# Optimization experiments

Measured on AMD Instinct MI355X. Metric: run time of the kernel, lower is better.

## Reference

```python
import jax, jax.numpy as jnp
import numpy as np

FP8_MAX = 448.0
EPS = 1e-12


def setup_inputs() -> dict:
    key = jax.random.key(0)
    k1, k2 = jax.random.split(key)
    x = jax.random.normal(k1, (4, 2048, 4096), dtype=jnp.float32)
    # kaiming-uniform-like init scale for weight
    weight = jax.random.normal(k2, (4096, 4096), dtype=jnp.float32) * 0.02
    bias = jnp.zeros((4096,), dtype=jnp.float32)
    return {"x": x, "weight": weight, "bias": bias}


def reference(x, weight, bias):
    # per-tensor fake-quant of activations
    input_scale = jnp.maximum(jnp.max(jnp.abs(x)) / FP8_MAX, EPS)
    x_q = jnp.round(jnp.clip(x / input_scale, -FP8_MAX, FP8_MAX))
    # per-tensor fake-quant of weight
    weight_scale = jnp.maximum(jnp.max(jnp.abs(weight)) / FP8_MAX, EPS)
    weight_q = jnp.round(jnp.clip(weight / weight_scale, -FP8_MAX, FP8_MAX))
    # GEMM in quantized domain, then dequant rescale + bias
    out_q = jnp.einsum('bsi,oi->bso', x_q, weight_q)  # [B,S,out]
    out = (out_q * (input_scale * weight_scale)).astype(x.dtype) + bias
    return out
```

## Files before the change

kernel.cpp:

```cpp
#include <hip/hip_runtime.h>

#define FP8_MAX 448.0f
#define EPSF 1e-12f

#define BM 256
#define BN 256
#define BK 64

typedef __attribute__((ext_vector_type(8))) _Float16 half8;
typedef __attribute__((ext_vector_type(4))) float floatx4;

__device__ inline void async_copy16(const void* gp, void* lp) {
  __builtin_amdgcn_global_load_lds(
      (const __attribute__((address_space(1))) unsigned int*)gp,
      (__attribute__((address_space(3))) unsigned int*)lp,
      16, 0, 0);
}

__global__ void absmax_kernel(const float* __restrict__ in, int n4,
                              unsigned* __restrict__ out) {
  int tid = blockIdx.x * blockDim.x + threadIdx.x;
  int stride = gridDim.x * blockDim.x;
  const float4* in4 = (const float4*)in;
  float m = 0.f;
  for (int i = tid; i < n4; i += stride) {
    float4 v = in4[i];
    m = fmaxf(m, fmaxf(fmaxf(fabsf(v.x), fabsf(v.y)),
                       fmaxf(fabsf(v.z), fabsf(v.w))));
  }
  for (int off = 32; off > 0; off >>= 1)
    m = fmaxf(m, __shfl_down(m, off, 64));
  __shared__ float smax[4];
  int lane = threadIdx.x & 63, w = threadIdx.x >> 6;
  if (lane == 0) smax[w] = m;
  __syncthreads();
  if (threadIdx.x == 0) {
    float b = fmaxf(fmaxf(smax[0], smax[1]), fmaxf(smax[2], smax[3]));
    atomicMax(out, __float_as_uint(b));
  }
}

__global__ void quant_kernel(const float* __restrict__ in,
                             _Float16* __restrict__ out, int n8,
                             const unsigned* __restrict__ amax_bits) {
  const float scale = fmaxf(__uint_as_float(*amax_bits) / FP8_MAX, EPSF);
  int tid = blockIdx.x * blockDim.x + threadIdx.x;
  int stride = gridDim.x * blockDim.x;
  const float4* in4 = (const float4*)in;
  half8* out8 = (half8*)out;
  for (int i = tid; i < n8; i += stride) {
    float4 a = in4[2 * i], b = in4[2 * i + 1];
    half8 h;
    h[0] = (_Float16)rintf(fminf(fmaxf(a.x / scale, -FP8_MAX), FP8_MAX));
    h[1] = (_Float16)rintf(fminf(fmaxf(a.y / scale, -FP8_MAX), FP8_MAX));
    h[2] = (_Float16)rintf(fminf(fmaxf(a.z / scale, -FP8_MAX), FP8_MAX));
    h[3] = (_Float16)rintf(fminf(fmaxf(a.w / scale, -FP8_MAX), FP8_MAX));
    h[4] = (_Float16)rintf(fminf(fmaxf(b.x / scale, -FP8_MAX), FP8_MAX));
    h[5] = (_Float16)rintf(fminf(fmaxf(b.y / scale, -FP8_MAX), FP8_MAX));
    h[6] = (_Float16)rintf(fminf(fmaxf(b.z / scale, -FP8_MAX), FP8_MAX));
    h[7] = (_Float16)rintf(fminf(fmaxf(b.w / scale, -FP8_MAX), FP8_MAX));
    out8[i] = h;
  }
}

__global__ __launch_bounds__(512, 2) void gemm8_kernel(
    const _Float16* __restrict__ A,
    const _Float16* __restrict__ B,
    const float* __restrict__ bias, const unsigned* __restrict__ amax,
    float* __restrict__ C,
    int M, int N, int K) {
  __shared__ __align__(16) _Float16 As[2][BM * BK];
  __shared__ __align__(16) _Float16 Bs[2][BN * BK];

  const int tid = threadIdx.x;
  const int w = tid >> 6;
  const int lane = tid & 63;
  const int wr = w >> 2;
  const int wc = w & 3;

  const int nwg = gridDim.x;
  const int cpx = nwg >> 3;
  const int swz = (blockIdx.x & 7) * cpx + (blockIdx.x >> 3);
  const int nbn = N / BN;
  const int bm = swz / nbn;
  const int bn = swz % nbn;

  const _Float16* Ab = A + (size_t)bm * BM * K;
  const _Float16* Bb = B + (size_t)bn * BN * K;

  const int srow8 = w * 8 + (lane >> 3);
  const int gd8 = ((lane & 7) ^ ((lane >> 3) & 7)) * 8;
  const _Float16* Ag = Ab + (size_t)srow8 * K + gd8;
  const _Float16* Bg = Bb + (size_t)srow8 * K + gd8;

  auto stageA = [&](int kt, int h) {
#pragma unroll
    for (int r = 0; r < 2; ++r)
      async_copy16(Ag + (size_t)(h * 128 + r * 64) * K + kt * BK,
                   (void*)&As[kt & 1][(h * 128 + r * 64 + w * 8) * BK]);
  };
  auto stageB = [&](int kt, int h) {
#pragma unroll
    for (int r = 0; r < 2; ++r)
      async_copy16(Bg + (size_t)(h * 128 + r * 64) * K + kt * BK,
                   (void*)&Bs[kt & 1][(h * 128 + r * 64 + w * 8) * BK]);
  };

  const int lr = lane & 15;
  const int hi = lane >> 4;
  const int aoff = (wr * 128 + lr) * BK;
  const int boff = (wc * 64 + lr) * BK;
  const int g0 = ((hi) ^ (lr & 7)) * 8;
  const int g1 = ((4 + hi) ^ (lr & 7)) * 8;

  floatx4 acc[8][4] = {};
  const int nt = K / BK;

  stageA(0, 0); stageA(0, 1); stageB(0, 0); stageB(0, 1);
  stageA(1, 0); stageA(1, 1);
  asm volatile("s_waitcnt vmcnt(4)" ::: "memory");
  __builtin_amdgcn_s_barrier();

  for (int t = 0; t < nt; ++t) {
    const int b = t & 1;
    const _Float16* Asb = &As[b][0];
    const _Float16* Bsb = &Bs[b][0];
    half8 a_lo0[4], a_hi0[4], a_lo1[4], a_hi1[4], bf0[4], bf1[4];

#pragma unroll
    for (int m = 0; m < 4; ++m)
      a_lo0[m] = *(const half8*)&Asb[aoff + m * 16 * BK + g0];
#pragma unroll
    for (int n = 0; n < 4; ++n)
      bf0[n] = *(const half8*)&Bsb[boff + n * 16 * BK + g0];
    if (t + 1 < nt) stageB(t + 1, 0);
    __builtin_amdgcn_s_barrier();
    asm volatile("s_waitcnt lgkmcnt(0)");
    __builtin_amdgcn_s_setprio(1);
#pragma unroll
    for (int m = 0; m < 4; ++m)
#pragma unroll
      for (int n = 0; n < 4; ++n)
        acc[m][n] = __builtin_amdgcn_mfma_f32_16x16x32_f16(
            a_lo0[m], bf0[n], acc[m][n], 0, 0, 0);
    __builtin_amdgcn_s_setprio(0);
    __builtin_amdgcn_s_barrier();

#pragma unroll
    for (int m = 0; m < 4; ++m)
      a_hi0[m] = *(const half8*)&Asb[aoff + (64 + m * 16) * BK + g0];
#pragma unroll
    for (int n = 0; n < 4; ++n)
      bf1[n] = *(const half8*)&Bsb[boff + n * 16 * BK + g1];
    if (t + 1 < nt) stageB(t + 1, 1);
    __builtin_amdgcn_s_barrier();
    asm volatile("s_waitcnt lgkmcnt(0)");
    __builtin_amdgcn_s_setprio(1);
#pragma unroll
    for (int m = 0; m < 4; ++m)
#pragma unroll
      for (int n = 0; n < 4; ++n)
        acc[4 + m][n] = __builtin_amdgcn_mfma_f32_16x16x32_f16(
            a_hi0[m], bf0[n], acc[4 + m][n], 0, 0, 0);
    __builtin_amdgcn_s_setprio(0);
    __builtin_amdgcn_s_barrier();

#pragma unroll
    for (int m = 0; m < 4; ++m)
      a_lo1[m] = *(const half8*)&Asb[aoff + m * 16 * BK + g1];
#pragma unroll
    for (int m = 0; m < 4; ++m)
      a_hi1[m] = *(const half8*)&Asb[aoff + (64 + m * 16) * BK + g1];
    __builtin_amdgcn_s_barrier();
    asm volatile("s_waitcnt lgkmcnt(0)");
    __builtin_amdgcn_s_setprio(1);
#pragma unroll
    for (int m = 0; m < 4; ++m)
#pragma unroll
      for (int n = 0; n < 4; ++n)
        acc[m][n] = __builtin_amdgcn_mfma_f32_16x16x32_f16(
            a_lo1[m], bf1[n], acc[m][n], 0, 0, 0);
    __builtin_amdgcn_s_setprio(0);
    __builtin_amdgcn_s_barrier();

    __builtin_amdgcn_sched_barrier(0);
    if (t + 2 < nt) { stageA(t + 2, 0); stageA(t + 2, 1); }
    __builtin_amdgcn_s_barrier();
    __builtin_amdgcn_s_setprio(1);
#pragma unroll
    for (int m = 0; m < 4; ++m)
#pragma unroll
      for (int n = 0; n < 4; ++n)
        acc[4 + m][n] = __builtin_amdgcn_mfma_f32_16x16x32_f16(
            a_hi1[m], bf1[n], acc[4 + m][n], 0, 0, 0);
    __builtin_amdgcn_s_setprio(0);
    if (t + 2 < nt) {
      asm volatile("s_waitcnt vmcnt(4)" ::: "memory");
    } else {
      asm volatile("s_waitcnt vmcnt(0)" ::: "memory");
    }
    __builtin_amdgcn_s_barrier();
  }

  const float sx = fmaxf(__uint_as_float(amax[0]) / FP8_MAX, EPSF);
  const float sw = fmaxf(__uint_as_float(amax[1]) / FP8_MAX, EPSF);
  const float s = sx * sw;

  const int row0 = bm * BM + wr * 128 + hi * 4;
  const int col0 = bn * BN + wc * 64 + lr;
  float bv[4];
#pragma unroll
  for (int n = 0; n < 4; ++n) bv[n] = bias[col0 + n * 16];

#pragma unroll
  for (int m = 0; m < 8; ++m) {
#pragma unroll
    for (int n = 0; n < 4; ++n) {
      const size_t base = (size_t)(row0 + m * 16) * N + col0 + n * 16;
#pragma unroll
      for (int r = 0; r < 4; ++r)
        C[base + (size_t)r * N] = acc[m][n][r] * s + bv[n];
    }
  }
}

extern "C" void kernel_launch(void* const* d_in, const int* in_sizes, int n_in,
                              void* d_out, int out_size, void* d_ws,
                              size_t ws_size, hipStream_t stream) {
  const float* x = (const float*)d_in[0];
  const float* wgt = (const float*)d_in[1];
  const float* bias = (const float*)d_in[2];
  float* out = (float*)d_out;

  const int N = in_sizes[2];
  const int K = in_sizes[1] / N;
  const int M = in_sizes[0] / K;

  unsigned* amax = (unsigned*)d_ws;
  _Float16* xq = (_Float16*)((char*)d_ws + 256);
  _Float16* wq =
      (_Float16*)((char*)d_ws + 256 + (size_t)M * K * sizeof(_Float16));

  hipMemsetAsync(d_ws, 0, 8, stream);
  absmax_kernel<<<2048, 256, 0, stream>>>(x, M * K / 4, amax);
  absmax_kernel<<<1024, 256, 0, stream>>>(wgt, N * K / 4, amax + 1);
  quant_kernel<<<2048, 256, 0, stream>>>(x, xq, M * K / 8, amax);
  quant_kernel<<<1024, 256, 0, stream>>>(wgt, wq, N * K / 8, amax + 1);

  gemm8_kernel<<<dim3((M / BM) * (N / BN)), 512, 0, stream>>>(
      xq, wq, bias, amax, out, M, N, K);
}
```

Measured before the change: 408.4 us.

## Software-pipeline LDS fragment reads one phase ahead of MFMA clusters

Restructures the GEMM main loop so each phase's LDS fragment reads are issued before the preceding MFMA cluster and waited on with partial lgkmcnt counts, instead of loading then fully draining before each cluster. The next tile's first fragments are prefetched during the final MFMA phase, and the per-half staging calls are merged into single whole-tile issues. The intent is to hide LDS latency behind matrix math and remove some barrier round trips. This keeps more fragment registers live, which raises pressure, and it depends on the waitcnt counts and barrier placement being correct with respect to the double buffer.

```diff
diff --git a/kernel.cpp b/kernel.cpp
--- a/kernel.cpp
+++ b/kernel.cpp
@@ -9,6 +9,13 @@
 
 typedef __attribute__((ext_vector_type(8))) _Float16 half8;
 typedef __attribute__((ext_vector_type(4))) float floatx4;
+
+#define VMCNT(n) asm volatile("s_waitcnt vmcnt(" #n ")" ::: "memory")
+#define LGKM(n)                                       \
+  do {                                                \
+    asm volatile("s_waitcnt lgkmcnt(" #n ")" ::: "memory"); \
+    __builtin_amdgcn_sched_barrier(0);                \
+  } while (0)
 
 __device__ inline void async_copy16(const void* gp, void* lp) {
   __builtin_amdgcn_global_load_lds(
@@ -93,112 +100,116 @@
   const _Float16* Ag = Ab + (size_t)srow8 * K + gd8;
   const _Float16* Bg = Bb + (size_t)srow8 * K + gd8;
 
-  auto stageA = [&](int kt, int h) {
-#pragma unroll
-    for (int r = 0; r < 2; ++r)
-      async_copy16(Ag + (size_t)(h * 128 + r * 64) * K + kt * BK,
-                   (void*)&As[kt & 1][(h * 128 + r * 64 + w * 8) * BK]);
+  auto stageA = [&](int kt) {
+#pragma unroll
+    for (int r = 0; r < 4; ++r)
+      async_copy16(Ag + (size_t)(r * 64) * K + kt * BK,
+                   (void*)&As[kt & 1][(r * 64 + w * 8) * BK]);
   };
-  auto stageB = [&](int kt, int h) {
-#pragma unroll
-    for (int r = 0; r < 2; ++r)
-      async_copy16(Bg + (size_t)(h * 128 + r * 64) * K + kt * BK,
-                   (void*)&Bs[kt & 1][(h * 128 + r * 64 + w * 8) * BK]);
+  auto stageB = [&](int kt) {
+#pragma unroll
+    for (int r = 0; r < 4; ++r)
+      async_copy16(Bg + (size_t)(r * 64) * K + kt * BK,
+                   (void*)&Bs[kt & 1][(r * 64 + w * 8) * BK]);
   };
 
   const int lr = lane & 15;
   const int hi = lane >> 4;
   const int aoff = (wr * 128 + lr) * BK;
   const int boff = (wc * 64 + lr) * BK;
-  const int g0 = ((hi) ^ (lr & 7)) * 8;
+  const int g0 = (hi ^ (lr & 7)) * 8;
   const int g1 = ((4 + hi) ^ (lr & 7)) * 8;
 
+  half8 aL0[4], b0[4];
+  half8 aH0[4], b1[4];
+  half8 aL1[4], aH1[4];
   floatx4 acc[8][4] = {};
   const int nt = K / BK;
 
-  stageA(0, 0); stageA(0, 1); stageB(0, 0); stageB(0, 1);
-  stageA(1, 0); stageA(1, 1);
-  asm volatile("s_waitcnt vmcnt(4)" ::: "memory");
+  auto readR0 = [&](const _Float16* Asx, const _Float16* Bsx) {
+#pragma unroll
+    for (int m = 0; m < 4; ++m)
+      aL0[m] = *(const half8*)&Asx[aoff + m * 16 * BK + g0];
+#pragma unroll
+    for (int n = 0; n < 4; ++n)
+      b0[n] = *(const half8*)&Bsx[boff + n * 16 * BK + g0];
+  };
+
+  stageA(0);
+  stageB(0);
+  stageA(1);
+  VMCNT(4);
   __builtin_amdgcn_s_barrier();
+  readR0(&As[0][0], &Bs[0][0]);
 
   for (int t = 0; t < nt; ++t) {
     const int b = t & 1;
     const _Float16* Asb = &As[b][0];
     const _Float16* Bsb = &Bs[b][0];
-    half8 a_lo0[4], a_hi0[4], a_lo1[4], a_hi1[4], bf0[4], bf1[4];
-
-#pragma unroll
-    for (int m = 0; m < 4; ++m)
-      a_lo0[m] = *(const half8*)&Asb[aoff + m * 16 * BK + g0];
+
+    if (t + 1 < nt) stageB(t + 1);
+#pragma unroll
+    for (int m = 0; m < 4; ++m)
+      aH0[m] = *(const half8*)&Asb[aoff + (64 + m * 16) * BK + g0];
 #pragma unroll
     for (int n = 0; n < 4; ++n)
-      bf0[n] = *(const half8*)&Bsb[boff + n * 16 * BK + g0];
-    if (t + 1 < nt) stageB(t + 1, 0);
-    __builtin_amdgcn_s_barrier();
-    asm volatile("s_waitcnt lgkmcnt(0)");
+      b1[n] = *(const half8*)&Bsb[boff + n * 16 * BK + g1];
+    LGKM(8);
     __builtin_amdgcn_s_setprio(1);
 #pragma unroll
     for (int m = 0; m < 4; ++m)
 #pragma unroll
       for (int n = 0; n < 4; ++n)
         acc[m][n] = __builtin_amdgcn_mfma_f32_16x16x32_f16(
-            a_lo0[m], bf0[n], acc[m][n], 0, 0, 0);
-    __builtin_amdgcn_s_setprio(0);
-    __builtin_amdgcn_s_barrier();
-
-#pragma unroll
-    for (int m = 0; m < 4; ++m)
-      a_hi0[m] = *(const half8*)&Asb[aoff + (64 + m * 16) * BK + g0];
-#pragma unroll
-    for (int n = 0; n < 4; ++n)
-      bf1[n] = *(const half8*)&Bsb[boff + n * 16 * BK + g1];
-    if (t + 1 < nt) stageB(t + 1, 1);
-    __builtin_amdgcn_s_barrier();
-    asm volatile("s_waitcnt lgkmcnt(0)");
+            aL0[m], b0[n], acc[m][n], 0, 0, 0);
+    __builtin_amdgcn_s_setprio(0);
+    __builtin_amdgcn_s_barrier();
+
+#pragma unroll
+    for (int m = 0; m < 4; ++m)
+      aL1[m] = *(const half8*)&Asb[aoff + m * 16 * BK + g1];
+#pragma unroll
+    for (int m = 0; m < 4; ++m)
+      aH1[m] = *(const half8*)&Asb[aoff + (64 + m * 16) * BK + g1];
+    LGKM(8);
     __builtin_amdgcn_s_setprio(1);
 #pragma unroll
     for (int m = 0; m < 4; ++m)
 #pragma unroll
       for (int n = 0; n < 4; ++n)
         acc[4 + m][n] = __builtin_amdgcn_mfma_f32_16x16x32_f16(
-            a_hi0[m], bf0[n], acc[4 + m][n], 0, 0, 0);
-    __builtin_amdgcn_s_setprio(0);
-    __builtin_amdgcn_s_barrier();
-
-#pragma unroll
-    for (int m = 0; m < 4; ++m)
-      a_lo1[m] = *(const half8*)&Asb[aoff + m * 16 * BK + g1];
-#pragma unroll
-    for (int m = 0; m < 4; ++m)
-      a_hi1[m] = *(const half8*)&Asb[aoff + (64 + m * 16) * BK + g1];
-    __builtin_amdgcn_s_barrier();
-    asm volatile("s_waitcnt lgkmcnt(0)");
+            aH0[m], b0[n], acc[4 + m][n], 0, 0, 0);
+    __builtin_amdgcn_s_setprio(0);
+    __builtin_amdgcn_s_barrier();
+
+    LGKM(0);
     __builtin_amdgcn_s_setprio(1);
 #pragma unroll
     for (int m = 0; m < 4; ++m)
 #pragma unroll
       for (int n = 0; n < 4; ++n)
         acc[m][n] = __builtin_amdgcn_mfma_f32_16x16x32_f16(
-            a_lo1[m], bf1[n], acc[m][n], 0, 0, 0);
-    __builtin_amdgcn_s_setprio(0);
-    __builtin_amdgcn_s_barrier();
-
+            aL1[m], b1[n], acc[m][n], 0, 0, 0);
+    __builtin_amdgcn_s_setprio(0);
+    __builtin_amdgcn_s_barrier();
+
+    if (t + 2 < nt) {
+      stageA(t + 2);
+      VMCNT(4);
+    } else {
+      VMCNT(0);
+    }
+    __builtin_amdgcn_s_barrier();
     __builtin_amdgcn_sched_barrier(0);
-    if (t + 2 < nt) { stageA(t + 2, 0); stageA(t + 2, 1); }
-    __builtin_amdgcn_s_barrier();
+    if (t + 1 < nt) readR0(&As[b ^ 1][0], &Bs[b ^ 1][0]);
     __builtin_amdgcn_s_setprio(1);
 #pragma unroll
     for (int m = 0; m < 4; ++m)
 #pragma unroll
       for (int n = 0; n < 4; ++n)
         acc[4 + m][n] = __builtin_amdgcn_mfma_f32_16x16x32_f16(
-            a_hi1[m], bf1[n], acc[4 + m][n], 0, 0, 0);
-    __builtin_amdgcn_s_setprio(0);
-    if (t + 2 < nt) {
-      asm volatile("s_waitcnt vmcnt(4)" ::: "memory");
-    } else {
-      asm volatile("s_waitcnt vmcnt(0)" ::: "memory");
-    }
+            aH1[m], b1[n], acc[4 + m][n], 0, 0, 0);
+    __builtin_amdgcn_s_setprio(0);
     __builtin_amdgcn_s_barrier();
   }
 
```

Measured after the change: 486.8 us. +19.2%, slower.

## Reorder GEMM k-loop into quadrant phases with full-K fragments and split A staging

Applied to the files above, without the earlier changes.

Restructures the GEMM main loop so each of its four phases computes one output quadrant (A low/high half times B low/high half) over both k-halves, loading each LDS fragment once per iteration. The A prefetch for tile t+2 is split across the last two phases instead of being issued in one burst. The stage lambdas now take the row chunk directly. The aim is fewer LDS reads and register fragments per step and better overlap of global loads with MFMA work. The risk is more live registers held across phases, and LDS reuse timing changes because the last two phases drop the lgkmcnt wait and barriers between loads and compute.

```diff
diff --git a/kernel.cpp b/kernel.cpp
--- a/kernel.cpp
+++ b/kernel.cpp
@@ -9,6 +9,8 @@
 
 typedef __attribute__((ext_vector_type(8))) _Float16 half8;
 typedef __attribute__((ext_vector_type(4))) float floatx4;
+
+#define VMCNT(n) asm volatile("s_waitcnt vmcnt(" #n ")" ::: "memory")
 
 __device__ inline void async_copy16(const void* gp, void* lp) {
   __builtin_amdgcn_global_load_lds(
@@ -95,109 +97,116 @@
 
   auto stageA = [&](int kt, int h) {
 #pragma unroll
-    for (int r = 0; r < 2; ++r)
-      async_copy16(Ag + (size_t)(h * 128 + r * 64) * K + kt * BK,
-                   (void*)&As[kt & 1][(h * 128 + r * 64 + w * 8) * BK]);
+    for (int r = 2 * h; r < 2 * h + 2; ++r)
+      async_copy16(Ag + (size_t)(r * 64) * K + kt * BK,
+                   (void*)&As[kt & 1][(r * 64 + w * 8) * BK]);
   };
   auto stageB = [&](int kt, int h) {
 #pragma unroll
-    for (int r = 0; r < 2; ++r)
-      async_copy16(Bg + (size_t)(h * 128 + r * 64) * K + kt * BK,
-                   (void*)&Bs[kt & 1][(h * 128 + r * 64 + w * 8) * BK]);
+    for (int r = 2 * h; r < 2 * h + 2; ++r)
+      async_copy16(Bg + (size_t)(r * 64) * K + kt * BK,
+                   (void*)&Bs[kt & 1][(r * 64 + w * 8) * BK]);
   };
 
   const int lr = lane & 15;
   const int hi = lane >> 4;
   const int aoff = (wr * 128 + lr) * BK;
   const int boff = (wc * 64 + lr) * BK;
-  const int g0 = ((hi) ^ (lr & 7)) * 8;
+  const int g0 = (hi ^ (lr & 7)) * 8;
   const int g1 = ((4 + hi) ^ (lr & 7)) * 8;
 
+  half8 aL[4][2], aH[4][2], bL[2][2], bH[2][2];
   floatx4 acc[8][4] = {};
   const int nt = K / BK;
 
   stageA(0, 0); stageA(0, 1); stageB(0, 0); stageB(0, 1);
   stageA(1, 0); stageA(1, 1);
-  asm volatile("s_waitcnt vmcnt(4)" ::: "memory");
+  VMCNT(4);
   __builtin_amdgcn_s_barrier();
 
   for (int t = 0; t < nt; ++t) {
     const int b = t & 1;
     const _Float16* Asb = &As[b][0];
     const _Float16* Bsb = &Bs[b][0];
-    half8 a_lo0[4], a_hi0[4], a_lo1[4], a_hi1[4], bf0[4], bf1[4];
-
-#pragma unroll
-    for (int m = 0; m < 4; ++m)
-      a_lo0[m] = *(const half8*)&Asb[aoff + m * 16 * BK + g0];
-#pragma unroll
-    for (int n = 0; n < 4; ++n)
-      bf0[n] = *(const half8*)&Bsb[boff + n * 16 * BK + g0];
+
+#pragma unroll
+    for (int m = 0; m < 4; ++m) {
+      aL[m][0] = *(const half8*)&Asb[aoff + m * 16 * BK + g0];
+      aL[m][1] = *(const half8*)&Asb[aoff + m * 16 * BK + g1];
+    }
+#pragma unroll
+    for (int n = 0; n < 2; ++n) {
+      bL[n][0] = *(const half8*)&Bsb[boff + n * 16 * BK + g0];
+      bL[n][1] = *(const half8*)&Bsb[boff + n * 16 * BK + g1];
+    }
     if (t + 1 < nt) stageB(t + 1, 0);
     __builtin_amdgcn_s_barrier();
-    asm volatile("s_waitcnt lgkmcnt(0)");
-    __builtin_amdgcn_s_setprio(1);
-#pragma unroll
-    for (int m = 0; m < 4; ++m)
-#pragma unroll
-      for (int n = 0; n < 4; ++n)
-        acc[m][n] = __builtin_amdgcn_mfma_f32_16x16x32_f16(
-            a_lo0[m], bf0[n], acc[m][n], 0, 0, 0);
-    __builtin_amdgcn_s_setprio(0);
-    __builtin_amdgcn_s_barrier();
-
-#pragma unroll
-    for (int m = 0; m < 4; ++m)
-      a_hi0[m] = *(const half8*)&Asb[aoff + (64 + m * 16) * BK + g0];
-#pragma unroll
-    for (int n = 0; n < 4; ++n)
-      bf1[n] = *(const half8*)&Bsb[boff + n * 16 * BK + g1];
+    asm volatile("s_waitcnt lgkmcnt(0)" ::: "memory");
+    __builtin_amdgcn_s_setprio(1);
+#pragma unroll
+    for (int m = 0; m < 4; ++m)
+#pragma unroll
+      for (int n = 0; n < 2; ++n)
+#pragma unroll
+        for (int kk = 0; kk < 2; ++kk)
+          acc[m][n] = __builtin_amdgcn_mfma_f32_16x16x32_f16(
+              aL[m][kk], bL[n][kk], acc[m][n], 0, 0, 0);
+    __builtin_amdgcn_s_setprio(0);
+    __builtin_amdgcn_s_barrier();
+
+#pragma unroll
+    for (int m = 0; m < 4; ++m) {
+      aH[m][0] = *(const half8*)&Asb[aoff + (64 + m * 16) * BK + g0];
+      aH[m][1] = *(const half8*)&Asb[aoff + (64 + m * 16) * BK + g1];
+    }
+#pragma unroll
+    for (int n = 0; n < 2; ++n) {
+      bH[n][0] = *(const half8*)&Bsb[boff + (32 + n * 16) * BK + g0];
+      bH[n][1] = *(const half8*)&Bsb[boff + (32 + n * 16) * BK + g1];
+    }
     if (t + 1 < nt) stageB(t + 1, 1);
     __builtin_amdgcn_s_barrier();
-    asm volatile("s_waitcnt lgkmcnt(0)");
-    __builtin_amdgcn_s_setprio(1);
-#pragma unroll
-    for (int m = 0; m < 4; ++m)
-#pragma unroll
-      for (int n = 0; n < 4; ++n)
-        acc[4 + m][n] = __builtin_amdgcn_mfma_f32_16x16x32_f16(
-            a_hi0[m], bf0[n], acc[4 + m][n], 0, 0, 0);
-    __builtin_amdgcn_s_setprio(0);
-    __builtin_amdgcn_s_barrier();
-
-#pragma unroll
-    for (int m = 0; m < 4; ++m)
-      a_lo1[m] = *(const half8*)&Asb[aoff + m * 16 * BK + g1];
-#pragma unroll
-    for (int m = 0; m < 4; ++m)
-      a_hi1[m] = *(const half8*)&Asb[aoff + (64 + m * 16) * BK + g1];
-    __builtin_amdgcn_s_barrier();
-    asm volatile("s_waitcnt lgkmcnt(0)");
-    __builtin_amdgcn_s_setprio(1);
-#pragma unroll
-    for (int m = 0; m < 4; ++m)
-#pragma unroll
-      for (int n = 0; n < 4; ++n)
-        acc[m][n] = __builtin_amdgcn_mfma_f32_16x16x32_f16(
-            a_lo1[m], bf1[n], acc[m][n], 0, 0, 0);
-    __builtin_amdgcn_s_setprio(0);
-    __builtin_amdgcn_s_barrier();
-
-    __builtin_amdgcn_sched_barrier(0);
-    if (t + 2 < nt) { stageA(t + 2, 0); stageA(t + 2, 1); }
-    __builtin_amdgcn_s_barrier();
-    __builtin_amdgcn_s_setprio(1);
-#pragma unroll
-    for (int m = 0; m < 4; ++m)
-#pragma unroll
-      for (int n = 0; n < 4; ++n)
-        acc[4 + m][n] = __builtin_amdgcn_mfma_f32_16x16x32_f16(
-            a_hi1[m], bf1[n], acc[4 + m][n], 0, 0, 0);
+    asm volatile("s_waitcnt lgkmcnt(0)" ::: "memory");
+    __builtin_amdgcn_s_setprio(1);
+#pragma unroll
+    for (int m = 0; m < 4; ++m)
+#pragma unroll
+      for (int n = 0; n < 2; ++n)
+#pragma unroll
+        for (int kk = 0; kk < 2; ++kk)
+          acc[m][2 + n] = __builtin_amdgcn_mfma_f32_16x16x32_f16(
+              aL[m][kk], bH[n][kk], acc[m][2 + n], 0, 0, 0);
+    __builtin_amdgcn_s_setprio(0);
+    __builtin_amdgcn_s_barrier();
+
+    if (t + 2 < nt) stageA(t + 2, 0);
+    __builtin_amdgcn_s_setprio(1);
+#pragma unroll
+    for (int m = 0; m < 4; ++m)
+#pragma unroll
+      for (int n = 0; n < 2; ++n)
+#pragma unroll
+        for (int kk = 0; kk < 2; ++kk)
+          acc[4 + m][n] = __builtin_amdgcn_mfma_f32_16x16x32_f16(
+              aH[m][kk], bL[n][kk], acc[4 + m][n], 0, 0, 0);
+    __builtin_amdgcn_s_setprio(0);
+    __builtin_amdgcn_s_barrier();
+
+    if (t + 2 < nt) stageA(t + 2, 1);
+    __builtin_amdgcn_s_setprio(1);
+#pragma unroll
+    for (int m = 0; m < 4; ++m)
+#pragma unroll
+      for (int n = 0; n < 2; ++n)
+#pragma unroll
+        for (int kk = 0; kk < 2; ++kk)
+          acc[4 + m][2 + n] = __builtin_amdgcn_mfma_f32_16x16x32_f16(
+              aH[m][kk], bH[n][kk], acc[4 + m][2 + n], 0, 0, 0);
     __builtin_amdgcn_s_setprio(0);
     if (t + 2 < nt) {
-      asm volatile("s_waitcnt vmcnt(4)" ::: "memory");
+      VMCNT(4);
     } else {
-      asm volatile("s_waitcnt vmcnt(0)" ::: "memory");
+      VMCNT(0);
     }
     __builtin_amdgcn_s_barrier();
   }
```

Result: faster. 395.6 us (-3.1%).
